# Kernel tuning notes

Hardware: AMD Instinct MI355X
Metric: run time of the kernel (lower is better)

Reference implementation:

```python
import jax, jax.numpy as jnp
import numpy as np

N_QUBITS = 8
N_LAYERS = 7


def setup_inputs() -> dict:
    key = jax.random.key(0)
    ks = jax.random.split(key, 6)
    B = 65536
    return {
        "x": jax.random.normal(ks[0], (B, 2 ** N_QUBITS), dtype=jnp.float32),
        "weights": jax.random.normal(ks[1], (N_LAYERS, N_QUBITS), dtype=jnp.float32),
        "W1": jax.random.normal(ks[2], (16, 1), dtype=jnp.float32) * 0.5,
        "b1": jax.random.normal(ks[3], (16,), dtype=jnp.float32) * 0.1,
        "W2": jax.random.normal(ks[4], (1, 16), dtype=jnp.float32) * 0.5,
        "b2": jax.random.normal(ks[5], (1,), dtype=jnp.float32) * 0.1,
    }


def _apply_ry(psi, q, theta):
    # RY(theta) = [[cos(t/2), -sin(t/2)], [sin(t/2), cos(t/2)]] on wire q (axis q+1)
    c = jnp.cos(theta * 0.5)
    s = jnp.sin(theta * 0.5)
    a = jnp.take(psi, 0, axis=q + 1)
    b = jnp.take(psi, 1, axis=q + 1)
    return jnp.stack([c * a - s * b, s * a + c * b], axis=q + 1)


def _apply_cnot(psi, q):
    # CNOT control=q, target=q+1: flip target amplitudes where control=1
    ctl0 = jnp.take(psi, 0, axis=q + 1)
    ctl1 = jnp.take(psi, 1, axis=q + 1)
    # after removing axis q+1, target wire q+1 sits at axis q+1 of the slice
    ctl1 = jnp.flip(ctl1, axis=q + 1)
    return jnp.stack([ctl0, ctl1], axis=q + 1)


def _circuit(x, weights):
    B = x.shape[0]
    # AmplitudeEmbedding(normalize=True): real input -> real state (RY, CNOT are real)
    psi = x / jnp.linalg.norm(x, axis=1, keepdims=True)
    psi = psi.reshape((B,) + (2,) * N_QUBITS)  # axis 1 == wire 0 (MSB)
    for l in range(N_LAYERS):
        for q in range(N_QUBITS):
            psi = _apply_ry(psi, q, weights[l, q])
        for q in range(N_QUBITS - 1):
            psi = _apply_cnot(psi, q)
    probs = (psi ** 2).reshape(B, 2, -1)
    # <PauliZ(0)> = P(wire0=0) - P(wire0=1)
    return jnp.sum(probs[:, 0] - probs[:, 1], axis=1)


def reference(x, weights, W1, b1, W2, b2):
    z = _circuit(x, weights)[:, None]          # [B, 1]
    h = jax.nn.relu(z @ W1.T + b1)             # [B, 16]
    return jax.nn.sigmoid(h @ W2.T + b2)       # [B, 1]
```

## Files before the change

kernel.cpp:

```cpp
#include <hip/hip_runtime.h>
#include <hip/hip_bf16.h>

typedef __attribute__((ext_vector_type(8))) short bf16x8;
typedef __attribute__((ext_vector_type(4))) float f32x4;

__device__ __forceinline__ unsigned short f2bf(float f) {
    unsigned u = __builtin_bit_cast(unsigned, f);
    unsigned rnd = 0x7FFFu + ((u >> 16) & 1u);
    return (unsigned short)((u + rnd) >> 16);
}

__device__ __forceinline__ void wg_barrier() {
    asm volatile("s_waitcnt lgkmcnt(0)" ::: "memory");
    __builtin_amdgcn_sched_barrier(0);
    __builtin_amdgcn_s_barrier();
    __builtin_amdgcn_sched_barrier(0);
}

__global__ __launch_bounds__(256) void qnn_setup(const float* __restrict__ wts,
                                                 unsigned short* __restrict__ Bp) {
    __shared__ float cs[56], sn[56];
    int tid = threadIdx.x;
    if (tid < 56) {
        float th = 0.5f * wts[tid];
        cs[tid] = cosf(th);
        sn[tid] = sinf(th);
    }
    __syncthreads();

    int l = tid & 63;
    int k = blockIdx.x * 4 + (tid >> 6);
    int a0 = l << 2;

    float v0 = (float)(a0 + 0 == k);
    float v1 = (float)(a0 + 1 == k);
    float v2 = (float)(a0 + 2 == k);
    float v3 = (float)(a0 + 3 == k);

#pragma unroll
    for (int L = 0; L < 7; ++L) {
#pragma unroll
        for (int q = 0; q <= 5; ++q) {
            int m = 5 - q;
            float c = cs[L * 8 + q], s = sn[L * 8 + q];
            float ss = ((l >> m) & 1) ? s : -s;
            float p0 = __shfl_xor(v0, 1 << m);
            float p1 = __shfl_xor(v1, 1 << m);
            float p2 = __shfl_xor(v2, 1 << m);
            float p3 = __shfl_xor(v3, 1 << m);
            v0 = fmaf(ss, p0, c * v0);
            v1 = fmaf(ss, p1, c * v1);
            v2 = fmaf(ss, p2, c * v2);
            v3 = fmaf(ss, p3, c * v3);
        }
        {
            float c = cs[L * 8 + 6], s = sn[L * 8 + 6];
            float n0 = fmaf(-s, v2, c * v0), n2 = fmaf(s, v0, c * v2);
            float n1 = fmaf(-s, v3, c * v1), n3 = fmaf(s, v1, c * v3);
            v0 = n0; v1 = n1; v2 = n2; v3 = n3;
        }
        {
            float c = cs[L * 8 + 7], s = sn[L * 8 + 7];
            float n0 = fmaf(-s, v1, c * v0), n1 = fmaf(s, v0, c * v1);
            float n2 = fmaf(-s, v3, c * v2), n3 = fmaf(s, v2, c * v3);
            v0 = n0; v1 = n1; v2 = n2; v3 = n3;
        }
        {
            int src = l;
#pragma unroll
            for (int q = 4; q >= 0; --q)
                src = src ^ (((src >> (5 - q)) & 1) << (4 - q));
            v0 = __shfl(v0, src);
            v1 = __shfl(v1, src);
            v2 = __shfl(v2, src);
            v3 = __shfl(v3, src);
        }
        {
            bool cc = (l & 1);
            float n0 = cc ? v2 : v0, n2 = cc ? v0 : v2;
            float n1 = cc ? v3 : v1, n3 = cc ? v1 : v3;
            v0 = n0; v1 = n1; v2 = n2; v3 = n3;
        }
        {
            float t = v2; v2 = v3; v3 = t;
        }
    }

    int t = k >> 5, j = k & 7, lk = (k >> 3) & 3;
#pragma unroll
    for (int r = 0; r < 4; ++r) {
        int n = a0 + r;
        int u = n >> 4;
        int ls = lk * 16 + (n & 15);
        float val = (r == 0) ? v0 : (r == 1) ? v1 : (r == 2) ? v2 : v3;
        Bp[(((u * 8 + t) * 64) + ls) * 8 + j] = f2bf(val);
    }
}

__device__ __forceinline__ void cvt_store(const float4& a, const float4& b,
                                          unsigned short (*Xp)[256],
                                          int sr, int qt) {
    bf16x8 h;
    h[0] = (short)f2bf(a.x); h[1] = (short)f2bf(a.y);
    h[2] = (short)f2bf(a.z); h[3] = (short)f2bf(a.w);
    h[4] = (short)f2bf(b.x); h[5] = (short)f2bf(b.y);
    h[6] = (short)f2bf(b.z); h[7] = (short)f2bf(b.w);
    *(bf16x8*)&Xp[sr][(qt ^ (sr & 7)) * 8] = h;
}

__global__ __launch_bounds__(512, 4) void qnn_main(
    const float* __restrict__ x, const unsigned short* __restrict__ Bp,
    const float* __restrict__ W1, const float* __restrict__ b1,
    const float* __restrict__ W2, const float* __restrict__ b2,
    float* __restrict__ out) {
    __shared__ __align__(16) unsigned short Xs[2][16][256];
    __shared__ float Qpart[8][64];

    int tid = threadIdx.x;
    int l = tid & 63, w = tid >> 6;
    int sr = tid >> 5, qt = tid & 31;
    size_t base = (size_t)blockIdx.x * 64 * 256;
    const float* xst = x + base + (size_t)sr * 256 + qt * 8;

    const unsigned short* up = Bp + (size_t)(2 * w) * 4096 + l * 8;
    bf16x8 uf0[8], uf1[8];
#pragma unroll
    for (int t = 0; t < 8; ++t) {
        uf0[t] = *(const bf16x8*)(up + t * 512);
        uf1[t] = *(const bf16x8*)(up + 4096 + t * 512);
    }

    float4 pf[2][2];
    pf[0][0] = *(const float4*)(xst);
    pf[0][1] = *(const float4*)(xst + 4);
    pf[1][0] = *(const float4*)(xst + 4096);
    pf[1][1] = *(const float4*)(xst + 4100);
    cvt_store(pf[0][0], pf[0][1], Xs[0], sr, qt);
    wg_barrier();

    int row = l & 15, kg = l >> 4;

#pragma unroll
    for (int t = 0; t < 4; ++t) {
        if (t + 2 < 4) {
            pf[t & 1][0] = *(const float4*)(xst + (size_t)(t + 2) * 4096);
            pf[t & 1][1] = *(const float4*)(xst + (size_t)(t + 2) * 4096 + 4);
        }
        {
            const unsigned short* rp = &Xs[t & 1][row][0];
            f32x4 a0 = {0.f, 0.f, 0.f, 0.f}, a1 = {0.f, 0.f, 0.f, 0.f};
#pragma unroll
            for (int ks = 0; ks < 8; ++ks) {
                bf16x8 xf = *(const bf16x8*)(rp + (((ks << 2) | kg) ^ (row & 7)) * 8);
                a0 = __builtin_amdgcn_mfma_f32_16x16x32_bf16(uf0[ks], xf, a0, 0, 0, 0);
                a1 = __builtin_amdgcn_mfma_f32_16x16x32_bf16(uf1[ks], xf, a1, 0, 0, 0);
            }
            float q = 0.f;
#pragma unroll
            for (int j = 0; j < 4; ++j)
                q = fmaf(a0[j], a0[j], fmaf(a1[j], a1[j], q));
            q += __shfl_xor(q, 16);
            q += __shfl_xor(q, 32);
            if (l < 16) Qpart[w][t * 16 + l] = q;
        }
        if (t + 1 < 4)
            cvt_store(pf[(t + 1) & 1][0], pf[(t + 1) & 1][1],
                      Xs[(t + 1) & 1], sr, qt);
        wg_barrier();
    }

    if (tid < 64) {
        float pp = Qpart[0][tid] + Qpart[1][tid] + Qpart[2][tid] + Qpart[3][tid];
        float pm = Qpart[4][tid] + Qpart[5][tid] + Qpart[6][tid] + Qpart[7][tid];
        float z = (pp - pm) / (pp + pm);
        float o = b2[0];
#pragma unroll
        for (int jj = 0; jj < 16; ++jj) {
            float h = fmaf(z, W1[jj], b1[jj]);
            h = h > 0.f ? h : 0.f;
            o = fmaf(W2[jj], h, o);
        }
        out[(size_t)blockIdx.x * 64 + tid] = 1.f / (1.f + expf(-o));
    }
}

extern "C" void kernel_launch(void* const* d_in, const int* in_sizes, int n_in,
                              void* d_out, int out_size, void* d_ws, size_t ws_size,
                              hipStream_t stream) {
    const float* x   = (const float*)d_in[0];
    const float* wts = (const float*)d_in[1];
    const float* W1  = (const float*)d_in[2];
    const float* b1  = (const float*)d_in[3];
    const float* W2  = (const float*)d_in[4];
    const float* b2  = (const float*)d_in[5];
    float* out = (float*)d_out;
    unsigned short* Bp = (unsigned short*)d_ws;

    int B = in_sizes[0] >> 8;
    qnn_setup<<<64, 256, 0, stream>>>(wts, Bp);
    qnn_main<<<B / 64, 512, 0, stream>>>(x, Bp, W1, b1, W2, b2, out);
}
```

Before: 23.88 us.

## Use orthogonality to compute only the wire-0=1 half and normalize by input norm

Since the circuit is orthogonal, total probability equals the squared input norm. Each wave now computes only the second half of the output amplitudes (the rows with wire0=1), which halves the MFMA count and the register footprint for the unitary. The input norm comes from a shuffle reduction in fp32 during the bf16 conversion, and z is computed as 1 - 2*pm/norm. This mixes fp32 norms with bf16-computed projections, which may shift accuracy slightly. Occupancy in the launch bounds rises from 4 to 6 to exploit the lower register use.

```diff
diff --git a/kernel.cpp b/kernel.cpp
--- a/kernel.cpp
+++ b/kernel.cpp
@@ -99,22 +99,31 @@
 
 __device__ __forceinline__ void cvt_store(const float4& a, const float4& b,
                                           unsigned short (*Xp)[256],
-                                          int sr, int qt) {
+                                          float* NrmT, int sr, int qt) {
+    float ss = fmaf(a.x, a.x, fmaf(a.y, a.y, fmaf(a.z, a.z, a.w * a.w)));
+    ss = fmaf(b.x, b.x, fmaf(b.y, b.y, fmaf(b.z, b.z, fmaf(b.w, b.w, ss))));
     bf16x8 h;
     h[0] = (short)f2bf(a.x); h[1] = (short)f2bf(a.y);
     h[2] = (short)f2bf(a.z); h[3] = (short)f2bf(a.w);
     h[4] = (short)f2bf(b.x); h[5] = (short)f2bf(b.y);
     h[6] = (short)f2bf(b.z); h[7] = (short)f2bf(b.w);
     *(bf16x8*)&Xp[sr][(qt ^ (sr & 7)) * 8] = h;
-}
-
-__global__ __launch_bounds__(512, 4) void qnn_main(
+    ss += __shfl_xor(ss, 1);
+    ss += __shfl_xor(ss, 2);
+    ss += __shfl_xor(ss, 4);
+    ss += __shfl_xor(ss, 8);
+    ss += __shfl_xor(ss, 16);
+    if (qt == 0) NrmT[sr] = ss;
+}
+
+__global__ __launch_bounds__(512, 6) void qnn_main(
     const float* __restrict__ x, const unsigned short* __restrict__ Bp,
     const float* __restrict__ W1, const float* __restrict__ b1,
     const float* __restrict__ W2, const float* __restrict__ b2,
     float* __restrict__ out) {
     __shared__ __align__(16) unsigned short Xs[2][16][256];
     __shared__ float Qpart[8][64];
+    __shared__ float Nrm[64];
 
     int tid = threadIdx.x;
     int l = tid & 63, w = tid >> 6;
@@ -122,20 +131,17 @@
     size_t base = (size_t)blockIdx.x * 64 * 256;
     const float* xst = x + base + (size_t)sr * 256 + qt * 8;
 
-    const unsigned short* up = Bp + (size_t)(2 * w) * 4096 + l * 8;
-    bf16x8 uf0[8], uf1[8];
-#pragma unroll
-    for (int t = 0; t < 8; ++t) {
-        uf0[t] = *(const bf16x8*)(up + t * 512);
-        uf1[t] = *(const bf16x8*)(up + 4096 + t * 512);
-    }
+    const unsigned short* up = Bp + (size_t)(8 + w) * 4096 + l * 8;
+    bf16x8 uf[8];
+#pragma unroll
+    for (int t = 0; t < 8; ++t) uf[t] = *(const bf16x8*)(up + t * 512);
 
     float4 pf[2][2];
     pf[0][0] = *(const float4*)(xst);
     pf[0][1] = *(const float4*)(xst + 4);
     pf[1][0] = *(const float4*)(xst + 4096);
     pf[1][1] = *(const float4*)(xst + 4100);
-    cvt_store(pf[0][0], pf[0][1], Xs[0], sr, qt);
+    cvt_store(pf[0][0], pf[0][1], Xs[0], Nrm, sr, qt);
     wg_barrier();
 
     int row = l & 15, kg = l >> 4;
@@ -148,31 +154,29 @@
         }
         {
             const unsigned short* rp = &Xs[t & 1][row][0];
-            f32x4 a0 = {0.f, 0.f, 0.f, 0.f}, a1 = {0.f, 0.f, 0.f, 0.f};
+            f32x4 a0 = {0.f, 0.f, 0.f, 0.f};
 #pragma unroll
             for (int ks = 0; ks < 8; ++ks) {
                 bf16x8 xf = *(const bf16x8*)(rp + (((ks << 2) | kg) ^ (row & 7)) * 8);
-                a0 = __builtin_amdgcn_mfma_f32_16x16x32_bf16(uf0[ks], xf, a0, 0, 0, 0);
-                a1 = __builtin_amdgcn_mfma_f32_16x16x32_bf16(uf1[ks], xf, a1, 0, 0, 0);
+                a0 = __builtin_amdgcn_mfma_f32_16x16x32_bf16(uf[ks], xf, a0, 0, 0, 0);
             }
             float q = 0.f;
 #pragma unroll
-            for (int j = 0; j < 4; ++j)
-                q = fmaf(a0[j], a0[j], fmaf(a1[j], a1[j], q));
+            for (int j = 0; j < 4; ++j) q = fmaf(a0[j], a0[j], q);
             q += __shfl_xor(q, 16);
             q += __shfl_xor(q, 32);
             if (l < 16) Qpart[w][t * 16 + l] = q;
         }
         if (t + 1 < 4)
             cvt_store(pf[(t + 1) & 1][0], pf[(t + 1) & 1][1],
-                      Xs[(t + 1) & 1], sr, qt);
+                      Xs[(t + 1) & 1], Nrm + (t + 1) * 16, sr, qt);
         wg_barrier();
     }
 
     if (tid < 64) {
-        float pp = Qpart[0][tid] + Qpart[1][tid] + Qpart[2][tid] + Qpart[3][tid];
-        float pm = Qpart[4][tid] + Qpart[5][tid] + Qpart[6][tid] + Qpart[7][tid];
-        float z = (pp - pm) / (pp + pm);
+        float pm = Qpart[0][tid] + Qpart[1][tid] + Qpart[2][tid] + Qpart[3][tid]
+                 + Qpart[4][tid] + Qpart[5][tid] + Qpart[6][tid] + Qpart[7][tid];
+        float z = 1.f - 2.f * pm / Nrm[tid];
         float o = b2[0];
 #pragma unroll
         for (int jj = 0; jj < 16; ++jj) {
```

Result: faster. 22.69 us (median of 2 runs) (-5.0%).
